# Optimization experiments

Hardware: AMD Instinct MI355X
Metric: run time of the kernel (lower is better)

## Reference

```python
import jax, jax.numpy as jnp
import numpy as np

HIDDEN = 1024
HEADS = 16
HEAD_DIM = HIDDEN // HEADS


def setup_inputs() -> dict:
    key = jax.random.key(0)
    ks = jax.random.split(key, 9)
    B, S = 4, 2048
    s = 1.0 / np.sqrt(HIDDEN)
    return {
        "inputs": jax.random.normal(ks[0], (B, S, HIDDEN), dtype=jnp.float32),
        "Wq": jax.random.normal(ks[1], (HIDDEN, HIDDEN), dtype=jnp.float32) * s,
        "bq": jnp.zeros((HIDDEN,), dtype=jnp.float32),
        "Wk": jax.random.normal(ks[2], (HIDDEN, HIDDEN), dtype=jnp.float32) * s,
        "bk": jnp.zeros((HIDDEN,), dtype=jnp.float32),
        "Wv": jax.random.normal(ks[3], (HIDDEN, HIDDEN), dtype=jnp.float32) * s,
        "bv": jnp.zeros((HIDDEN,), dtype=jnp.float32),
        "Wp": jax.random.normal(ks[4], (HIDDEN, HIDDEN), dtype=jnp.float32) * s,
        "bp": jnp.zeros((HIDDEN,), dtype=jnp.float32),
        "heads_z": jnp.ones((1, HEADS, 1, 1), dtype=jnp.float32),
        "hidden_z": jnp.ones((HIDDEN,), dtype=jnp.float32),
    }


def _split_heads(x):
    # [B,S,HIDDEN] -> [B,H,S,Dh]
    B, S, _ = x.shape
    return x.reshape(B, S, HEADS, HEAD_DIM).transpose(0, 2, 1, 3)


def reference(inputs, Wq, bq, Wk, bk, Wv, bv, Wp, bp, heads_z, hidden_z):
    q = _split_heads(inputs @ Wq.T + bq)
    k = _split_heads(inputs @ Wk.T + bk)
    v = _split_heads(inputs @ Wv.T + bv)
    scores = jnp.einsum("bhqd,bhkd->bhqk", q, k) / jnp.sqrt(
        jnp.asarray(HEAD_DIM, dtype=q.dtype))
    probs = jax.nn.softmax(scores, axis=-1)
    ctx = jnp.einsum("bhqk,bhkd->bhqd", probs, v)  # [B,H,S,Dh]
    ctx = ctx * heads_z
    B, H, S, D = ctx.shape
    ctx = ctx.transpose(0, 2, 1, 3).reshape(B, S, H * D)
    out = ctx @ Wp.T + bp
    out = out * hidden_z
    return out
```

## Files before the change

kernel.cpp:

```cpp
#include <hip/hip_runtime.h>
#include <hip/hip_bf16.h>

#define HID 1024
#define NH 16
#define DH 64
#define SEQ 2048
#define NB 4
#define MTOT (NB*SEQ)
#define SM_SCALE 0.18033688f

typedef __attribute__((ext_vector_type(4))) float f32x4;
typedef __attribute__((ext_vector_type(16))) float f32x16;
typedef __attribute__((ext_vector_type(8))) __bf16 bf16x8;
typedef __attribute__((ext_vector_type(4))) __bf16 bf16x4;
typedef __attribute__((ext_vector_type(2))) __bf16 bf16x2;
typedef __attribute__((ext_vector_type(2))) int i32x2;

__device__ __forceinline__ f32x4 mfma16(bf16x8 a, bf16x8 b, f32x4 c) {
    return __builtin_amdgcn_mfma_f32_16x16x32_bf16(a, b, c, 0, 0, 0);
}
__device__ __forceinline__ f32x16 mfma32(bf16x8 a, bf16x8 b, f32x16 c) {
    return __builtin_amdgcn_mfma_f32_32x32x16_bf16(a, b, c, 0, 0, 0);
}

__device__ __forceinline__ void gload16(const void* g, void* l) {
    __builtin_amdgcn_global_load_lds(
        (const __attribute__((address_space(1))) unsigned int*)g,
        (__attribute__((address_space(3))) unsigned int*)l, 16, 0, 0);
}

__device__ __forceinline__ float fexp2(float x) {
#if __has_builtin(__builtin_amdgcn_exp2f)
    return __builtin_amdgcn_exp2f(x);
#else
    return exp2f(x);
#endif
}

__device__ __forceinline__ unsigned pkbf2(float lo, float hi) {
    union { bf16x2 v; unsigned u; } c;
    c.v = (bf16x2){ (__bf16)lo, (__bf16)hi };
    return c.u;
}

__device__ __forceinline__ void swap32(unsigned &a, unsigned &b) {
#if __has_builtin(__builtin_amdgcn_permlane32_swap)
    i32x2 r = __builtin_amdgcn_permlane32_swap((int)a, (int)b, false, false);
    a = (unsigned)r.x; b = (unsigned)r.y;
#else
    const bool hi = (threadIdx.x & 32) != 0;
    unsigned ta = __shfl_xor(a, 32), tb = __shfl_xor(b, 32);
    unsigned na = hi ? tb : a;
    unsigned nb = hi ? b : ta;
    a = na; b = nb;
#endif
}

__global__ __launch_bounds__(256)
void cvt5(const float* __restrict__ X,  const float* __restrict__ Wq,
          const float* __restrict__ Wk, const float* __restrict__ Wv,
          const float* __restrict__ Wp,
          __bf16* __restrict__ Xb,  __bf16* __restrict__ Wqb,
          __bf16* __restrict__ Wkb, __bf16* __restrict__ Wvb,
          __bf16* __restrict__ Wpb)
{
    const float* src; __bf16* dst; int n;
    switch (blockIdx.y) {
        case 0:  src = X;  dst = Xb;  n = MTOT * HID; break;
        case 1:  src = Wq; dst = Wqb; n = HID * HID;  break;
        case 2:  src = Wk; dst = Wkb; n = HID * HID;  break;
        case 3:  src = Wv; dst = Wvb; n = HID * HID;  break;
        default: src = Wp; dst = Wpb; n = HID * HID;  break;
    }
    const int stride = gridDim.x * 256 * 4;
    for (int i = (blockIdx.x * 256 + threadIdx.x) * 4; i < n; i += stride) {
        float4 v = *(const float4*)(src + i);
        bf16x4 o = { (__bf16)v.x, (__bf16)v.y, (__bf16)v.z, (__bf16)v.w };
        *(bf16x4*)(dst + i) = o;
    }
}

template<int PROJ>
__global__ __launch_bounds__(512, 1)
void gemm8(const __bf16* __restrict__ A,
           const __bf16* __restrict__ Wq, const __bf16* __restrict__ Wk,
           const __bf16* __restrict__ Wv,
           const float* __restrict__ bq, const float* __restrict__ bk,
           const float* __restrict__ bv, const float* __restrict__ hz,
           __bf16* __restrict__ Qo, __bf16* __restrict__ Ko,
           __bf16* __restrict__ Vo, float* __restrict__ Po)
{
    __shared__ __bf16 As[3][256 * 64];
    __shared__ __bf16 Bs[3][128 * 64];
    const int tid = threadIdx.x, lane = tid & 63, wid = tid >> 6;
    const int m0 = blockIdx.x * 256, n0 = blockIdx.y * 128;
    const int wr = wid >> 1, wc = wid & 1;
    const int mode = PROJ ? 3 : (int)blockIdx.z;

    const __bf16* W    = PROJ ? Wq : (mode == 0 ? Wq : mode == 1 ? Wk : Wv);
    const float*  bias = PROJ ? bq : (mode == 0 ? bq : mode == 1 ? bk : bv);

    const int cA0 = tid, cA1 = tid + 512, cA2 = tid + 1024, cA3 = tid + 1536;
    const int cB0 = tid, cB1 = tid + 512;
    const __bf16* aA0 = A + (size_t)(m0 + (cA0 >> 3)) * HID + ((cA0 & 7) ^ ((cA0 >> 3) & 7)) * 8;
    const __bf16* aA1 = A + (size_t)(m0 + (cA1 >> 3)) * HID + ((cA1 & 7) ^ ((cA1 >> 3) & 7)) * 8;
    const __bf16* aA2 = A + (size_t)(m0 + (cA2 >> 3)) * HID + ((cA2 & 7) ^ ((cA2 >> 3) & 7)) * 8;
    const __bf16* aA3 = A + (size_t)(m0 + (cA3 >> 3)) * HID + ((cA3 & 7) ^ ((cA3 >> 3) & 7)) * 8;
    const __bf16* bB0 = W + (size_t)(n0 + (cB0 >> 3)) * HID + ((cB0 & 7) ^ ((cB0 >> 3) & 7)) * 8;
    const __bf16* bB1 = W + (size_t)(n0 + (cB1 >> 3)) * HID + ((cB1 & 7) ^ ((cB1 >> 3) & 7)) * 8;

#define STAGE_A(sl, j) do { char* d_ = (char*)&As[sl][0]; int kk_ = (j) * 64; \
    gload16(aA0 + kk_, d_ + cA0 * 16); gload16(aA1 + kk_, d_ + cA1 * 16);     \
    gload16(aA2 + kk_, d_ + cA2 * 16); gload16(aA3 + kk_, d_ + cA3 * 16); } while (0)
#define STAGE_B(sl, j) do { char* d_ = (char*)&Bs[sl][0]; int kk_ = (j) * 64; \
    gload16(bB0 + kk_, d_ + cB0 * 16); gload16(bB1 + kk_, d_ + cB1 * 16); } while (0)

    f32x4 acc[4][4];
    #pragma unroll
    for (int i = 0; i < 4; i++)
        #pragma unroll
        for (int j = 0; j < 4; j++) acc[i][j] = (f32x4){0.f, 0.f, 0.f, 0.f};

    const int la = lane & 15, lk = lane >> 4;

    STAGE_A(0, 0); STAGE_B(0, 0);
    STAGE_A(1, 1); STAGE_B(1, 1);
    asm volatile("s_waitcnt vmcnt(6)" ::: "memory");
    __builtin_amdgcn_s_barrier();

    int slc = 0;
    for (int j = 0; j < 16; ++j) {
        const char* Ab = (const char*)&As[slc][0];
        const char* Bb = (const char*)&Bs[slc][0];
        const int js = j + 2;
        const int sls = slc == 0 ? 2 : slc - 1;

        bf16x8 af[4][2], bf0[2][2];
        #pragma unroll
        for (int mi = 0; mi < 4; mi++)
            #pragma unroll
            for (int ks = 0; ks < 2; ks++) {
                int row = wr * 64 + mi * 16 + la;
                af[mi][ks] = *(const bf16x8*)(Ab + row * 128 +
                    ((ks * 64 + lk * 16) ^ ((row & 7) << 4)));
            }
        #pragma unroll
        for (int ni = 0; ni < 2; ni++)
            #pragma unroll
            for (int ks = 0; ks < 2; ks++) {
                int row = wc * 64 + ni * 16 + la;
                bf0[ni][ks] = *(const bf16x8*)(Bb + row * 128 +
                    ((ks * 64 + lk * 16) ^ ((row & 7) << 4)));
            }
        if (js < 16) STAGE_A(sls, js);
        __builtin_amdgcn_s_barrier();
        asm volatile("s_waitcnt lgkmcnt(0)" ::: "memory");
        __builtin_amdgcn_sched_barrier(0);
        __builtin_amdgcn_s_setprio(1);
        #pragma unroll
        for (int mi = 0; mi < 4; mi++)
            #pragma unroll
            for (int ni = 0; ni < 2; ni++) {
                acc[mi][ni] = mfma16(af[mi][0], bf0[ni][0], acc[mi][ni]);
                acc[mi][ni] = mfma16(af[mi][1], bf0[ni][1], acc[mi][ni]);
            }
        __builtin_amdgcn_s_setprio(0);
        __builtin_amdgcn_s_barrier();

        bf16x8 bf1[2][2];
        #pragma unroll
        for (int ni = 0; ni < 2; ni++)
            #pragma unroll
            for (int ks = 0; ks < 2; ks++) {
                int row = wc * 64 + (ni + 2) * 16 + la;
                bf1[ni][ks] = *(const bf16x8*)(Bb + row * 128 +
                    ((ks * 64 + lk * 16) ^ ((row & 7) << 4)));
            }
        if (js < 16) STAGE_B(sls, js);
        __builtin_amdgcn_s_barrier();
        asm volatile("s_waitcnt lgkmcnt(0)" ::: "memory");
        __builtin_amdgcn_sched_barrier(0);
        __builtin_amdgcn_s_setprio(1);
        #pragma unroll
        for (int mi = 0; mi < 4; mi++)
            #pragma unroll
            for (int ni = 0; ni < 2; ni++) {
                acc[mi][ni + 2] = mfma16(af[mi][0], bf1[ni][0], acc[mi][ni + 2]);
                acc[mi][ni + 2] = mfma16(af[mi][1], bf1[ni][1], acc[mi][ni + 2]);
            }
        __builtin_amdgcn_s_setprio(0);

        if (j < 13)       { asm volatile("s_waitcnt vmcnt(6)" ::: "memory"); }
        else if (j == 14) { asm volatile("s_waitcnt vmcnt(0)" ::: "memory"); }
        __builtin_amdgcn_s_barrier();

        slc = slc == 2 ? 0 : slc + 1;
    }
#undef STAGE_A
#undef STAGE_B

    if (PROJ) {
        #pragma unroll
        for (int mi = 0; mi < 4; mi++)
            #pragma unroll
            for (int ni = 0; ni < 4; ni++)
                #pragma unroll
                for (int r = 0; r < 4; r++) {
                    int m = m0 + wr * 64 + mi * 16 + lk * 4 + r;
                    int n = n0 + wc * 64 + ni * 16 + la;
                    Po[(size_t)m * HID + n] = (acc[mi][ni][r] + bias[n]) * hz[n];
                }
    } else if (mode == 2) {
        #pragma unroll
        for (int mi = 0; mi < 4; mi++)
            #pragma unroll
            for (int ni = 0; ni < 4; ni++) {
                int m = m0 + wr * 64 + mi * 16 + lk * 4;
                int n = n0 + wc * 64 + ni * 16 + la;
                int b = m >> 11, s = m & (SEQ - 1);
                int h = n >> 6,  d = n & 63;
                bf16x4 o;
                #pragma unroll
                for (int r = 0; r < 4; r++) o[r] = (__bf16)(acc[mi][ni][r] + bias[n]);
                *(bf16x4*)(Vo + ((size_t)(b * NH + h) * DH + d) * SEQ + s) = o;
            }
    } else {
        const float qs = (mode == 0) ? SM_SCALE : 1.0f;
        __bf16* Og = (mode == 0) ? Qo : Ko;
        #pragma unroll
        for (int mi = 0; mi < 4; mi++)
            #pragma unroll
            for (int ni = 0; ni < 4; ni++)
                #pragma unroll
                for (int r = 0; r < 4; r++) {
                    int m = m0 + wr * 64 + mi * 16 + lk * 4 + r;
                    int n = n0 + wc * 64 + ni * 16 + la;
                    float v = (acc[mi][ni][r] + bias[n]) * qs;
                    int b = m >> 11, s = m & (SEQ - 1);
                    int h = n >> 6,  d = n & 63;
                    Og[((size_t)(b * NH + h) * SEQ + s) * DH + d] = (__bf16)v;
                }
    }
}

#define KVB 128

__global__ __launch_bounds__(512, 4)
void attn(const __bf16* __restrict__ Q, const __bf16* __restrict__ K,
          const __bf16* __restrict__ VT, const float* __restrict__ heads_z,
          __bf16* __restrict__ C)
{
    __shared__ __bf16 Ks[2][64 * 128];
    __shared__ __bf16 Vs[2][64 * 128];
    const int tid = threadIdx.x, lane = tid & 63, wid = tid >> 6;
    const int lh = lane >> 5;
    const int id = blockIdx.x;
    const int bh = (id & 7) | ((id >> 6) << 3);
    const int qb = (id >> 3) & 7;
    const int b = bh >> 4, hd = bh & 15;
    const __bf16* Qg = Q + (size_t)bh * SEQ * DH;
    const __bf16* Kg = K + (size_t)bh * SEQ * DH;
    const __bf16* Vg = VT + (size_t)bh * DH * SEQ;
    const int q = qb * 256 + wid * 32 + (lane & 31);
    const int r0 = lane & 31;
    const int kx = (r0 & 15) << 4;

    bf16x8 ones8;
    #pragma unroll
    for (int j = 0; j < 8; j++) ones8[j] = (__bf16)1.0f;

    bf16x8 qf[4];
    #pragma unroll
    for (int s = 0; s < 4; s++)
        qf[s] = *(const bf16x8*)(Qg + (size_t)q * DH + s * 16 + lh * 8);

    f32x16 ctx0, ctx1;
    #pragma unroll
    for (int r = 0; r < 16; r++) { ctx0[r] = 0.f; ctx1[r] = 0.f; }
    float lrun = 0.f;

    const int kr = tid >> 4;
    const int ks = (tid & 15) ^ (kr & 15);
    const int kda = (ks & 7) * 8;
    const int kvA = kr + ((ks >> 3) << 6);
    const int kvB = kvA + 32;

#define STAGE(buf, kv0_) do {                                                         \
    char* dk_ = (char*)&Ks[buf][0]; char* dv_ = (char*)&Vs[buf][0];                   \
    gload16(Kg + (size_t)((kv0_) + kvA) * DH + kda, dk_ + tid * 16);                  \
    gload16(Kg + (size_t)((kv0_) + kvB) * DH + kda, dk_ + tid * 16 + 8192);           \
    gload16(Vg + (size_t)kr * SEQ + (kv0_) + ks * 8, dv_ + tid * 16);                 \
    gload16(Vg + (size_t)(kr + 32) * SEQ + (kv0_) + ks * 8, dv_ + tid * 16 + 8192);   \
} while (0)

    STAGE(0, 0);
    __syncthreads();

    int cur = 0;
    for (int kv0 = 0; kv0 < SEQ; kv0 += KVB) {
        if (kv0 + KVB < SEQ) STAGE(cur ^ 1, kv0 + KVB);

        #pragma unroll
        for (int hh = 0; hh < 2; hh++) {
            const char* Kb = (const char*)&Ks[cur][0];
            const char* Vb = (const char*)&Vs[cur][0];

            f32x16 st0, st1;
            #pragma unroll
            for (int r = 0; r < 16; r++) { st0[r] = 0.f; st1[r] = 0.f; }
            __builtin_amdgcn_s_setprio(1);
            #pragma unroll
            for (int s = 0; s < 4; s++) {
                int co = (((hh * 8 + 2 * s + lh) << 4)) ^ kx;
                bf16x8 k0 = *(const bf16x8*)(Kb + r0 * 256 + co);
                bf16x8 k1 = *(const bf16x8*)(Kb + (r0 + 32) * 256 + co);
                st0 = mfma32(k0, qf[s], st0);
                st1 = mfma32(k1, qf[s], st1);
            }
            __builtin_amdgcn_s_setprio(0);

            #pragma unroll
            for (int r = 0; r < 16; r++) {
                st0[r] = fexp2(st0[r]);
                st1[r] = fexp2(st1[r]);
            }

            unsigned X0 = pkbf2(st0[0],  st0[1]),  X1 = pkbf2(st0[2],  st0[3]);
            unsigned X2 = pkbf2(st0[4],  st0[5]),  X3 = pkbf2(st0[6],  st0[7]);
            unsigned X4 = pkbf2(st0[8],  st0[9]),  X5 = pkbf2(st0[10], st0[11]);
            unsigned X6 = pkbf2(st0[12], st0[13]), X7 = pkbf2(st0[14], st0[15]);
            unsigned Y0 = pkbf2(st1[0],  st1[1]),  Y1 = pkbf2(st1[2],  st1[3]);
            unsigned Y2 = pkbf2(st1[4],  st1[5]),  Y3 = pkbf2(st1[6],  st1[7]);
            unsigned Y4 = pkbf2(st1[8],  st1[9]),  Y5 = pkbf2(st1[10], st1[11]);
            unsigned Y6 = pkbf2(st1[12], st1[13]), Y7 = pkbf2(st1[14], st1[15]);
            swap32(X0, X2); swap32(X1, X3);
            swap32(X4, X6); swap32(X5, X7);
            swap32(Y0, Y2); swap32(Y1, Y3);
            swap32(Y4, Y6); swap32(Y5, Y7);
            union W4 { unsigned w[4]; bf16x8 v; };
            W4 pf[4];
            pf[0].w[0]=X0; pf[0].w[1]=X1; pf[0].w[2]=X2; pf[0].w[3]=X3;
            pf[1].w[0]=X4; pf[1].w[1]=X5; pf[1].w[2]=X6; pf[1].w[3]=X7;
            pf[2].w[0]=Y0; pf[2].w[1]=Y1; pf[2].w[2]=Y2; pf[2].w[3]=Y3;
            pf[3].w[0]=Y4; pf[3].w[1]=Y5; pf[3].w[2]=Y6; pf[3].w[3]=Y7;

            st0[0] = 0.f;
            #pragma unroll
            for (int s = 0; s < 4; s++) st0 = mfma32(ones8, pf[s].v, st0);

            __builtin_amdgcn_s_setprio(1);
            #pragma unroll
            for (int s = 0; s < 4; s++) {
                int co = (((hh * 8 + 2 * s + lh) << 4)) ^ kx;
                bf16x8 v0 = *(const bf16x8*)(Vb + r0 * 256 + co);
                bf16x8 v1 = *(const bf16x8*)(Vb + (r0 + 32) * 256 + co);
                ctx0 = mfma32(v0, pf[s].v, ctx0);
                ctx1 = mfma32(v1, pf[s].v, ctx1);
            }
            __builtin_amdgcn_s_setprio(0);

            lrun += st0[0];
        }

        __syncthreads();
        cur ^= 1;
    }
#undef STAGE

    const float hzv = heads_z[hd];
    const float rl = hzv / lrun;
    __bf16* Crow = C + (size_t)(b * SEQ + q) * HID + hd * DH;
    #pragma unroll
    for (int g = 0; g < 4; g++) {
        bf16x4 o0, o1;
        #pragma unroll
        for (int j = 0; j < 4; j++) {
            o0[j] = (__bf16)(ctx0[4 * g + j] * rl);
            o1[j] = (__bf16)(ctx1[4 * g + j] * rl);
        }
        int d0 = 8 * g + 4 * lh;
        *(bf16x4*)(Crow + d0) = o0;
        *(bf16x4*)(Crow + 32 + d0) = o1;
    }
}

extern "C" void kernel_launch(void* const* d_in, const int* in_sizes, int n_in,
                              void* d_out, int out_size, void* d_ws, size_t ws_size,
                              hipStream_t stream)
{
    const float* X    = (const float*)d_in[0];
    const float* Wq   = (const float*)d_in[1];
    const float* bq   = (const float*)d_in[2];
    const float* Wk   = (const float*)d_in[3];
    const float* bk   = (const float*)d_in[4];
    const float* Wv   = (const float*)d_in[5];
    const float* bv   = (const float*)d_in[6];
    const float* Wp   = (const float*)d_in[7];
    const float* bp   = (const float*)d_in[8];
    const float* hz   = (const float*)d_in[9];
    const float* hidz = (const float*)d_in[10];

    __bf16* ws  = (__bf16*)d_ws;
    __bf16* Xb  = ws;
    __bf16* Wqb = Xb  + (size_t)MTOT * HID;
    __bf16* Wkb = Wqb + (size_t)HID * HID;
    __bf16* Wvb = Wkb + (size_t)HID * HID;
    __bf16* Wpb = Wvb + (size_t)HID * HID;
    __bf16* Qb  = Wpb + (size_t)HID * HID;
    __bf16* Kb  = Qb  + (size_t)MTOT * HID;
    __bf16* VTb = Kb  + (size_t)MTOT * HID;
    __bf16* Cb  = VTb + (size_t)MTOT * HID;

    cvt5<<<dim3(2048, 5), 256, 0, stream>>>(X, Wq, Wk, Wv, Wp, Xb, Wqb, Wkb, Wvb, Wpb);

    gemm8<0><<<dim3(MTOT / 256, HID / 128, 3), 512, 0, stream>>>(
        Xb, Wqb, Wkb, Wvb, bq, bk, bv, nullptr, Qb, Kb, VTb, nullptr);

    attn<<<dim3(512), 512, 0, stream>>>(Qb, Kb, VTb, hz, Cb);

    gemm8<1><<<dim3(MTOT / 256, HID / 128), 512, 0, stream>>>(
        Cb, Wpb, nullptr, nullptr, bp, nullptr, nullptr, hidz,
        nullptr, nullptr, nullptr, (float*)d_out);
}
```

Before: 187.5 us.

## Merge split GEMM k-loop phases into one and widen bf16 conversion stores

The GEMM main loop previously split each k-step into two halves, each with its own LDS reads, global staging, barriers and MFMA burst. Now it reads all A and B fragments at once, issues the A and B global-to-LDS stages together, and runs all 32 MFMAs in one burst, dropping two barriers per iteration. This cuts synchronisation overhead but raises register pressure and removes the finer interleaving of memory and compute. The fp32-to-bf16 conversion kernel also now handles 8 elements per thread with 16-byte stores.

```diff
diff --git a/kernel.cpp b/kernel.cpp
--- a/kernel.cpp
+++ b/kernel.cpp
@@ -72,11 +72,13 @@
         case 3:  src = Wv; dst = Wvb; n = HID * HID;  break;
         default: src = Wp; dst = Wpb; n = HID * HID;  break;
     }
-    const int stride = gridDim.x * 256 * 4;
-    for (int i = (blockIdx.x * 256 + threadIdx.x) * 4; i < n; i += stride) {
-        float4 v = *(const float4*)(src + i);
-        bf16x4 o = { (__bf16)v.x, (__bf16)v.y, (__bf16)v.z, (__bf16)v.w };
-        *(bf16x4*)(dst + i) = o;
+    const int stride = gridDim.x * 256 * 8;
+    for (int i = (blockIdx.x * 256 + threadIdx.x) * 8; i < n; i += stride) {
+        float4 v0 = *(const float4*)(src + i);
+        float4 v1 = *(const float4*)(src + i + 4);
+        bf16x8 o = { (__bf16)v0.x, (__bf16)v0.y, (__bf16)v0.z, (__bf16)v0.w,
+                     (__bf16)v1.x, (__bf16)v1.y, (__bf16)v1.z, (__bf16)v1.w };
+        *(bf16x8*)(dst + i) = o;
     }
 }
 
@@ -109,11 +111,11 @@
     const __bf16* bB0 = W + (size_t)(n0 + (cB0 >> 3)) * HID + ((cB0 & 7) ^ ((cB0 >> 3) & 7)) * 8;
     const __bf16* bB1 = W + (size_t)(n0 + (cB1 >> 3)) * HID + ((cB1 & 7) ^ ((cB1 >> 3) & 7)) * 8;
 
-#define STAGE_A(sl, j) do { char* d_ = (char*)&As[sl][0]; int kk_ = (j) * 64; \
-    gload16(aA0 + kk_, d_ + cA0 * 16); gload16(aA1 + kk_, d_ + cA1 * 16);     \
-    gload16(aA2 + kk_, d_ + cA2 * 16); gload16(aA3 + kk_, d_ + cA3 * 16); } while (0)
-#define STAGE_B(sl, j) do { char* d_ = (char*)&Bs[sl][0]; int kk_ = (j) * 64; \
-    gload16(bB0 + kk_, d_ + cB0 * 16); gload16(bB1 + kk_, d_ + cB1 * 16); } while (0)
+#define STAGE_AB(sl, j) do { char* da_ = (char*)&As[sl][0]; char* db_ = (char*)&Bs[sl][0]; \
+    int kk_ = (j) * 64;                                                                    \
+    gload16(aA0 + kk_, da_ + cA0 * 16); gload16(aA1 + kk_, da_ + cA1 * 16);                \
+    gload16(aA2 + kk_, da_ + cA2 * 16); gload16(aA3 + kk_, da_ + cA3 * 16);                \
+    gload16(bB0 + kk_, db_ + cB0 * 16); gload16(bB1 + kk_, db_ + cB1 * 16); } while (0)
 
     f32x4 acc[4][4];
     #pragma unroll
@@ -123,8 +125,8 @@
 
     const int la = lane & 15, lk = lane >> 4;
 
-    STAGE_A(0, 0); STAGE_B(0, 0);
-    STAGE_A(1, 1); STAGE_B(1, 1);
+    STAGE_AB(0, 0);
+    STAGE_AB(1, 1);
     asm volatile("s_waitcnt vmcnt(6)" ::: "memory");
     __builtin_amdgcn_s_barrier();
 
@@ -135,7 +137,7 @@
         const int js = j + 2;
         const int sls = slc == 0 ? 2 : slc - 1;
 
-        bf16x8 af[4][2], bf0[2][2];
+        bf16x8 af[4][2], bf[4][2];
         #pragma unroll
         for (int mi = 0; mi < 4; mi++)
             #pragma unroll
@@ -145,48 +147,25 @@
                     ((ks * 64 + lk * 16) ^ ((row & 7) << 4)));
             }
         #pragma unroll
-        for (int ni = 0; ni < 2; ni++)
+        for (int ni = 0; ni < 4; ni++)
             #pragma unroll
             for (int ks = 0; ks < 2; ks++) {
                 int row = wc * 64 + ni * 16 + la;
-                bf0[ni][ks] = *(const bf16x8*)(Bb + row * 128 +
+                bf[ni][ks] = *(const bf16x8*)(Bb + row * 128 +
                     ((ks * 64 + lk * 16) ^ ((row & 7) << 4)));
             }
-        if (js < 16) STAGE_A(sls, js);
-        __builtin_amdgcn_s_barrier();
+
+        if (js < 16) STAGE_AB(sls, js);
+
         asm volatile("s_waitcnt lgkmcnt(0)" ::: "memory");
         __builtin_amdgcn_sched_barrier(0);
         __builtin_amdgcn_s_setprio(1);
         #pragma unroll
         for (int mi = 0; mi < 4; mi++)
             #pragma unroll
-            for (int ni = 0; ni < 2; ni++) {
-                acc[mi][ni] = mfma16(af[mi][0], bf0[ni][0], acc[mi][ni]);
-                acc[mi][ni] = mfma16(af[mi][1], bf0[ni][1], acc[mi][ni]);
-            }
-        __builtin_amdgcn_s_setprio(0);
-        __builtin_amdgcn_s_barrier();
-
-        bf16x8 bf1[2][2];
-        #pragma unroll
-        for (int ni = 0; ni < 2; ni++)
-            #pragma unroll
-            for (int ks = 0; ks < 2; ks++) {
-                int row = wc * 64 + (ni + 2) * 16 + la;
-                bf1[ni][ks] = *(const bf16x8*)(Bb + row * 128 +
-                    ((ks * 64 + lk * 16) ^ ((row & 7) << 4)));
-            }
-        if (js < 16) STAGE_B(sls, js);
-        __builtin_amdgcn_s_barrier();
-        asm volatile("s_waitcnt lgkmcnt(0)" ::: "memory");
-        __builtin_amdgcn_sched_barrier(0);
-        __builtin_amdgcn_s_setprio(1);
-        #pragma unroll
-        for (int mi = 0; mi < 4; mi++)
-            #pragma unroll
-            for (int ni = 0; ni < 2; ni++) {
-                acc[mi][ni + 2] = mfma16(af[mi][0], bf1[ni][0], acc[mi][ni + 2]);
-                acc[mi][ni + 2] = mfma16(af[mi][1], bf1[ni][1], acc[mi][ni + 2]);
+            for (int ni = 0; ni < 4; ni++) {
+                acc[mi][ni] = mfma16(af[mi][0], bf[ni][0], acc[mi][ni]);
+                acc[mi][ni] = mfma16(af[mi][1], bf[ni][1], acc[mi][ni]);
             }
         __builtin_amdgcn_s_setprio(0);
 
@@ -196,8 +175,7 @@
 
         slc = slc == 2 ? 0 : slc + 1;
     }
-#undef STAGE_A
-#undef STAGE_B
+#undef STAGE_AB
 
     if (PROJ) {
         #pragma unroll
```

After: 178.5 us. -4.8%, faster.
